# Optimization experiments

Measured on AMD Instinct MI355X. Metric: run time of the kernel, lower is better.

## Reference

```python
import jax, jax.numpy as jnp
import numpy as np

N = 100000   # nodes
E = 400000   # edges
G = 2048     # graphs in batch
H = 128      # hidden_channels
V = 100      # in_channels (element vocab)
L = 3        # hidden_layers (GAT)
LO = 2       # out_layers (dense)
SLOPE = 0.2  # GATConv negative_slope default


def setup_inputs() -> dict:
    key = jax.random.key(0)
    ks = jax.random.split(key, 14)
    s = 1.0 / np.sqrt(H)
    return {
        "x": jax.random.randint(ks[0], (N,), 0, V),
        "edge_index": jax.random.randint(ks[1], (2, E), 0, N),
        "edge_attr": jax.random.uniform(ks[2], (E, 1), dtype=jnp.float32),
        "batch": jnp.sort(jax.random.randint(ks[3], (N,), 0, G)),
        "emb": jax.random.normal(ks[4], (V, H), dtype=jnp.float32),
        "gat_W": jax.random.normal(ks[5], (L, H, H), dtype=jnp.float32) * s,
        "att_src": jax.random.normal(ks[6], (L, H), dtype=jnp.float32) * s,
        "att_dst": jax.random.normal(ks[7], (L, H), dtype=jnp.float32) * s,
        "edge_W": jax.random.normal(ks[8], (L, H), dtype=jnp.float32) * s,  # lin_edge: Linear(1, H, bias=False)
        "att_edge": jax.random.normal(ks[9], (L, H), dtype=jnp.float32) * s,
        "gat_b": jnp.zeros((L, H), dtype=jnp.float32),
        "lin_W": jax.random.normal(ks[10], (LO, H, H), dtype=jnp.float32) * s,
        "lin_b": jnp.zeros((LO, H), dtype=jnp.float32),
        "wp_W": jax.random.normal(ks[11], (H, 1), dtype=jnp.float32) * s,
        "wp_b": jnp.zeros((1,), dtype=jnp.float32),
    }


def _segment_softmax(logits, seg, num_segments):
    m = jax.ops.segment_max(logits, seg, num_segments=num_segments)
    e = jnp.exp(logits - m[seg])
    s = jax.ops.segment_sum(e, seg, num_segments=num_segments)
    return e / s[seg]


def reference(x, edge_index, edge_attr, batch, emb, gat_W, att_src, att_dst,
              edge_W, att_edge, gat_b, lin_W, lin_b, wp_W, wp_b):
    src, dst = edge_index[0], edge_index[1]
    # GATConv add_self_loops=True with fill_value='mean' for edge_attr
    loop = jnp.arange(N, dtype=src.dtype)
    src_sl = jnp.concatenate([src, loop])          # [E+N]
    dst_sl = jnp.concatenate([dst, loop])          # [E+N]
    ea_mean = jnp.mean(edge_attr, axis=0, keepdims=True)  # [1,1]
    ea_sl = jnp.concatenate([edge_attr, jnp.broadcast_to(ea_mean, (N, 1))], axis=0)  # [E+N,1]

    h = emb[x]  # [N,H]
    for l in range(L):
        xt = h @ gat_W[l]                 # shared lin_src/lin_dst, heads=1
        a_s = xt @ att_src[l]             # [N]
        a_d = xt @ att_dst[l]             # [N]
        a_e = (ea_sl * edge_W[l][None, :]) @ att_edge[l]  # lin_edge then att_edge: [E+N]
        alpha = jax.nn.leaky_relu(a_s[src_sl] + a_d[dst_sl] + a_e, negative_slope=SLOPE)
        alpha = _segment_softmax(alpha, dst_sl, N)
        out = jax.ops.segment_sum(xt[src_sl] * alpha[:, None], dst_sl, num_segments=N)
        out = out + gat_b[l]
        # F.normalize(h_x, 2, dim=1)
        nrm = jnp.linalg.norm(out, axis=1, keepdims=True)
        h = out / jnp.maximum(nrm, 1e-12)
    for i in range(LO):
        h = jax.nn.relu(h @ lin_W[i] + lin_b[i])
    m_x = jax.ops.segment_sum(h, batch, num_segments=G)  # scatter_sum readout [G,H]
    props = m_x @ wp_W + wp_b                            # [G,1]
    return jnp.squeeze(props, axis=1)                    # [G]
```

## Files before the change

### kernel.cpp

```cpp
#include <hip/hip_runtime.h>
#include <math.h>

#define N_NODES 100000
#define N_EDGES 400000
#define NG 2048
#define H 128
#define NV 100
#define NLAYERS 3
#define SLOPE 0.2f

#define SCAL_N 64

typedef __attribute__((ext_vector_type(8))) short bf16x8;
typedef __attribute__((ext_vector_type(4))) float f32x4;

__device__ __forceinline__ float wave_reduce_sum(float v){
  #pragma unroll
  for (int off = 32; off > 0; off >>= 1) v += __shfl_xor(v, off, 64);
  return v;
}
__device__ __forceinline__ unsigned short rne_bf16(float f){
  unsigned int u = __float_as_uint(f);
  u += 0x7FFF + ((u >> 16) & 1);
  return (unsigned short)(u >> 16);
}

#define PB_CONVW 320
#define PB_CONVE (PB_CONVW + 50)
#define PB_OUT   (PB_CONVE + 8)
#define PB_DOTS  (PB_OUT + 1)
#define PB_EASUM (PB_DOTS + 256)
#define PB_DEG   (PB_EASUM + 1954)
__global__ __launch_bounds__(256) void k_prep(
    const float* __restrict__ gat_W, const float* __restrict__ lin_W,
    unsigned short* __restrict__ Wf,
    const float* __restrict__ emb, unsigned short* __restrict__ embb,
    const float* __restrict__ ea, const float* __restrict__ ew,
    const float* __restrict__ ae, float* __restrict__ scal,
    const float* __restrict__ wp_b, float* __restrict__ out,
    const int* __restrict__ ei, int* __restrict__ deg)
{
  int b = blockIdx.x, tid = threadIdx.x;
  if (b < PB_CONVW){
    int i = b*256 + tid;
    int m   = i >> 14;
    int r   = i & 16383;
    int k0i = r >> 12;
    int r3  = r & 4095;
    int ct  = r3 >> 9;
    int r4  = r3 & 511;
    int lane= r4 >> 3;
    int j   = r4 & 7;
    int q = lane >> 4, ln = lane & 15;
    int k = k0i*32 + q*8 + j;
    int n = ct*16 + ln;
    const float* src = (m < 3) ? (gat_W + m*16384) : (lin_W + (m-3)*16384);
    Wf[i] = rne_bf16(src[k*H + n]);
  } else if (b < PB_CONVE){
    int i = (b - PB_CONVW)*256 + tid;
    if (i < NV*H) embb[i] = rne_bf16(emb[i]);
  } else if (b < PB_OUT){
    int g = (b - PB_CONVE)*256 + tid;
    if (g < NG) out[g] = wp_b[0];
  } else if (b < PB_DOTS){
    int l = tid >> 6, ln = tid & 63;
    if (l < NLAYERS){
      float p = ew[l*H + ln]*ae[l*H + ln] + ew[l*H + ln + 64]*ae[l*H + ln + 64];
      p = wave_reduce_sum(p);
      if (ln == 0) atomicAdd(&scal[32 + l], p);
    }
  } else if (b < PB_EASUM){
    int i = (b - PB_DOTS)*256 + tid;
    int stride = 256*256;
    float v = 0.f;
    for (; i < N_EDGES; i += stride) v += ea[i];
    v = wave_reduce_sum(v);
    if ((tid & 63) == 0) atomicAdd(&scal[0], v);
  } else {
    int i = (b - PB_EASUM)*256 + tid;
    if (i < N_EDGES + N_NODES){
      int d = (i < N_EDGES) ? ei[N_EDGES + i] : (i - N_EDGES);
      atomicAdd(&deg[d], 1);
    }
  }
}

__global__ __launch_bounds__(256) void k_alloc(
    const int* __restrict__ deg, int* __restrict__ row_ptr, int* __restrict__ counter){
  __shared__ int wsum[4];
  __shared__ int base;
  int n = blockIdx.x * 256 + threadIdx.x;
  int d = (n < N_NODES) ? deg[n] : 0;
  int lane = threadIdx.x & 63, wid = threadIdx.x >> 6;
  int v = d;
  #pragma unroll
  for (int off = 1; off < 64; off <<= 1){
    int u = __shfl_up(v, off, 64);
    if (lane >= off) v += u;
  }
  if (lane == 63) wsum[wid] = v;
  __syncthreads();
  if (threadIdx.x == 0){
    int t0 = wsum[0], t1 = wsum[1], t2 = wsum[2], t3 = wsum[3];
    base = atomicAdd(counter, t0 + t1 + t2 + t3);
    wsum[0] = 0; wsum[1] = t0; wsum[2] = t0 + t1; wsum[3] = t0 + t1 + t2;
  }
  __syncthreads();
  if (n < N_NODES) row_ptr[n] = base + wsum[wid] + (v - d);
}

__global__ void k_scatter(const int* __restrict__ ei, const float* __restrict__ ea,
                          const float* __restrict__ scal, const int* __restrict__ row_ptr,
                          int* __restrict__ cursor, int* __restrict__ csr_src,
                          float* __restrict__ csr_ea){
  int i = blockIdx.x * blockDim.x + threadIdx.x;
  if (i >= N_EDGES + N_NODES) return;
  int s, d; float v;
  if (i < N_EDGES){ s = ei[i]; d = ei[N_EDGES + i]; v = ea[i]; }
  else            { s = d = i - N_EDGES; v = scal[0] * (1.0f / N_EDGES); }
  int pos = row_ptr[d] + atomicAdd(&cursor[d], 1);
  csr_src[pos] = s;
  csr_ea[pos]  = v;
}

__global__ __launch_bounds__(256, 4) void k_gemm(
    const unsigned short* __restrict__ Ab, const int* __restrict__ xmap,
    const unsigned short* __restrict__ Wf,
    unsigned short* __restrict__ Cb,
    const float* __restrict__ att1, const float* __restrict__ att2,
    float* __restrict__ a_s_out, float* __restrict__ a_d_out,
    const float* __restrict__ bias,
    const int* __restrict__ batch, float* __restrict__ out,
    int mode)
{
  __shared__ unsigned short lw[16384];
  int tid  = threadIdx.x;
  int w    = tid >> 6;
  int lane = tid & 63;
  int q    = lane >> 4;
  int ln   = lane & 15;
  int waveRow = blockIdx.x*128 + w*32;

  #pragma unroll
  for (int i = 0; i < 8; ++i){
    int base = (i*256 + w*64) * 8;
    __builtin_amdgcn_global_load_lds(
        (const __attribute__((address_space(1))) unsigned int*)(Wf + base + lane*8),
        (__attribute__((address_space(3))) unsigned int*)(lw + base),
        16, 0, 0);
  }

  bf16x8 af[2][4];
  #pragma unroll
  for (int m = 0; m < 2; ++m){
    int r = waveRow + m*16 + ln;
    if (r >= N_NODES) r = N_NODES - 1;
    if (xmap) r = xmap[r];
    const unsigned short* Ar = Ab + (size_t)r*H;
    #pragma unroll
    for (int k0i = 0; k0i < 4; ++k0i)
      af[m][k0i] = *(const bf16x8*)(Ar + k0i*32 + q*8);
  }
  __syncthreads();

  f32x4 acc[2][8];
  #pragma unroll
  for (int m = 0; m < 2; ++m)
    #pragma unroll
    for (int ct = 0; ct < 8; ++ct) acc[m][ct] = (f32x4){0.f,0.f,0.f,0.f};

  #pragma unroll
  for (int k0i = 0; k0i < 4; ++k0i){
    #pragma unroll
    for (int ct = 0; ct < 8; ++ct){
      bf16x8 bw = *(const bf16x8*)(lw + k0i*4096 + ct*512 + lane*8);
      #pragma unroll
      for (int m = 0; m < 2; ++m)
        acc[m][ct] = __builtin_amdgcn_mfma_f32_16x16x32_bf16(af[m][k0i], bw, acc[m][ct], 0,0,0);
    }
  }

  if (mode == 0){
    float as_l[8], ad_l[8];
    #pragma unroll
    for (int ct = 0; ct < 8; ++ct){ as_l[ct] = att1[ct*16+ln]; ad_l[ct] = att2[ct*16+ln]; }
    #pragma unroll
    for (int m = 0; m < 2; ++m){
      #pragma unroll
      for (int r = 0; r < 4; ++r){
        int grow = waveRow + m*16 + q*4 + r;
        bool ok = grow < N_NODES;
        float ps = 0.f, pd = 0.f;
        #pragma unroll
        for (int ct = 0; ct < 8; ++ct){
          float v = acc[m][ct][r];
          if (ok) Cb[(size_t)grow*H + ct*16 + ln] = rne_bf16(v);
          ps += v * as_l[ct]; pd += v * ad_l[ct];
        }
        #pragma unroll
        for (int mk = 8; mk > 0; mk >>= 1){
          ps += __shfl_xor(ps, mk, 64);
          pd += __shfl_xor(pd, mk, 64);
        }
        if (ok && ln == 0){ a_s_out[grow] = ps; a_d_out[grow] = pd; }
      }
    }
  } else if (mode == 1){
    float b_l[8];
    #pragma unroll
    for (int ct = 0; ct < 8; ++ct) b_l[ct] = bias[ct*16+ln];
    #pragma unroll
    for (int m = 0; m < 2; ++m){
      #pragma unroll
      for (int r = 0; r < 4; ++r){
        int grow = waveRow + m*16 + q*4 + r;
        if (grow >= N_NODES) continue;
        #pragma unroll
        for (int ct = 0; ct < 8; ++ct)
          Cb[(size_t)grow*H + ct*16 + ln] = rne_bf16(fmaxf(acc[m][ct][r] + b_l[ct], 0.f));
      }
    }
  } else {
    float b_l[8], wp_l[8];
    #pragma unroll
    for (int ct = 0; ct < 8; ++ct){ b_l[ct] = bias[ct*16+ln]; wp_l[ct] = att1[ct*16+ln]; }
    #pragma unroll
    for (int m = 0; m < 2; ++m){
      #pragma unroll
      for (int r = 0; r < 4; ++r){
        int grow = waveRow + m*16 + q*4 + r;
        bool ok = grow < N_NODES;
        float ps = 0.f;
        #pragma unroll
        for (int ct = 0; ct < 8; ++ct)
          ps += fmaxf(acc[m][ct][r] + b_l[ct], 0.f) * wp_l[ct];
        #pragma unroll
        for (int mk = 8; mk > 0; mk >>= 1) ps += __shfl_xor(ps, mk, 64);
        if (ok && ln == 0) atomicAdd(&out[batch[grow]], ps);
      }
    }
  }
}

__global__ __launch_bounds__(256, 4) void k_aggregate(
    const uint2* __restrict__ xtb2, const float* __restrict__ a_s,
    const float* __restrict__ a_d, const int* __restrict__ csr_src,
    const float* __restrict__ csr_ea, const int* __restrict__ row_ptr,
    const int* __restrict__ deg, const float* __restrict__ scal, int l,
    const float* __restrict__ bias, uint2* __restrict__ hb2)
{
  __shared__ int2 lsw[4][2][32];
  int wid  = threadIdx.x >> 6;
  int lane = threadIdx.x & 63;
  int h    = lane >> 5;
  int c    = lane & 31;
  int n    = blockIdx.x*8 + wid*2 + h;
  if (n >= N_NODES) return;
  int beg = row_ptr[n];
  int d   = deg[n];
  float adn = a_d[n];
  float dl  = scal[32 + l];
  int maxd = max(d, __shfl_xor(d, 32, 64));

  float4 acc = make_float4(0.f,0.f,0.f,0.f);
  float ss = 0.f;
  for (int base = 0; base < maxd; base += 32){
    int s = 0; float wgt = 0.f;
    int j = base + c;
    if (j < d){
      int e = beg + j;
      s = csr_src[e];
      float lg = a_s[s] + adn + dl*csr_ea[e];
      lg = (lg > 0.f) ? lg : SLOPE*lg;
      wgt = __expf(lg);
    }
    int2 pk; pk.x = s; pk.y = __float_as_int(wgt);
    lsw[wid][h][c] = pk;

    int cnt8 = (min(32, maxd - base) + 7) & ~7;
    for (int j0 = 0; j0 < cnt8; j0 += 8){
      int2 sw[8];
      #pragma unroll
      for (int u = 0; u < 8; ++u) sw[u] = lsw[wid][h][j0 + u];
      uint2 xv[8];
      #pragma unroll
      for (int u = 0; u < 8; ++u)
        xv[u] = xtb2[(size_t)sw[u].x*(H/4) + c];
      #pragma unroll
      for (int u = 0; u < 8; ++u){
        float wgt8 = __int_as_float(sw[u].y);
        float x0 = __uint_as_float(xv[u].x << 16);
        float x1 = __uint_as_float(xv[u].x & 0xFFFF0000u);
        float x2 = __uint_as_float(xv[u].y << 16);
        float x3 = __uint_as_float(xv[u].y & 0xFFFF0000u);
        ss    += wgt8;
        acc.x += wgt8 * x0;
        acc.y += wgt8 * x1;
        acc.z += wgt8 * x2;
        acc.w += wgt8 * x3;
      }
    }
  }

  float4 bv = *(const float4*)(bias + c*4);
  float inv = 1.0f / ss;
  acc.x = acc.x*inv + bv.x;
  acc.y = acc.y*inv + bv.y;
  acc.z = acc.z*inv + bv.z;
  acc.w = acc.w*inv + bv.w;
  float sq = acc.x*acc.x + acc.y*acc.y + acc.z*acc.z + acc.w*acc.w;
  #pragma unroll
  for (int off = 16; off > 0; off >>= 1) sq += __shfl_xor(sq, off, 64);
  float rn = 1.0f / fmaxf(sqrtf(sq), 1e-12f);
  uint2 o;
  o.x = ((unsigned int)rne_bf16(acc.y*rn) << 16) | rne_bf16(acc.x*rn);
  o.y = ((unsigned int)rne_bf16(acc.w*rn) << 16) | rne_bf16(acc.z*rn);
  hb2[(size_t)n*(H/4) + c] = o;
}

extern "C" void kernel_launch(void* const* d_in, const int* in_sizes, int n_in,
                              void* d_out, int out_size, void* d_ws, size_t ws_size,
                              hipStream_t stream) {
  const int*   x          = (const int*)  d_in[0];
  const int*   edge_index = (const int*)  d_in[1];
  const float* edge_attr  = (const float*)d_in[2];
  const int*   batch      = (const int*)  d_in[3];
  const float* emb        = (const float*)d_in[4];
  const float* gat_W      = (const float*)d_in[5];
  const float* att_src    = (const float*)d_in[6];
  const float* att_dst    = (const float*)d_in[7];
  const float* edge_W     = (const float*)d_in[8];
  const float* att_edge   = (const float*)d_in[9];
  const float* gat_b      = (const float*)d_in[10];
  const float* lin_W      = (const float*)d_in[11];
  const float* lin_b      = (const float*)d_in[12];
  const float* wp_W       = (const float*)d_in[13];
  const float* wp_b       = (const float*)d_in[14];
  float* out = (float*)d_out;

  unsigned short* hb  = (unsigned short*)d_ws;
  unsigned short* xtb = hb + (size_t)N_NODES*H;
  unsigned short* Wt  = xtb + (size_t)N_NODES*H;
  unsigned short* embb= Wt + 5*16384;
  float* a_s    = (float*)(embb + NV*H);
  float* a_d    = a_s + N_NODES;
  float* csr_ea = a_d + N_NODES;
  float* scal   = csr_ea + (N_EDGES + N_NODES);
  int*   deg    = (int*)(scal + SCAL_N);
  int*   cursor = deg + N_NODES;
  int*   row_ptr= cursor + N_NODES;
  int*   csr_src= row_ptr + N_NODES;

  hipMemsetAsync(scal, 0, (size_t)(SCAL_N + 2*N_NODES) * sizeof(float), stream);

  k_prep<<<PB_DEG, 256, 0, stream>>>(
      gat_W, lin_W, Wt, emb, embb, edge_attr, edge_W, att_edge, scal,
      wp_b, out, edge_index, deg);
  k_alloc<<<(N_NODES + 255)/256, 256, 0, stream>>>(deg, row_ptr, (int*)&scal[48]);
  k_scatter<<<(N_EDGES + N_NODES + 255)/256, 256, 0, stream>>>(
      edge_index, edge_attr, scal, row_ptr, cursor, csr_src, csr_ea);

  const int gemm_grid = (N_NODES + 127) / 128;
  for (int l = 0; l < NLAYERS; ++l){
    k_gemm<<<gemm_grid, 256, 0, stream>>>(
        (l == 0) ? embb : hb, (l == 0) ? x : nullptr,
        Wt + (size_t)l*16384, xtb,
        att_src + l*H, att_dst + l*H, a_s, a_d,
        nullptr, nullptr, nullptr, 0);
    k_aggregate<<<(N_NODES + 7)/8, 256, 0, stream>>>(
        (const uint2*)xtb, a_s, a_d, csr_src, csr_ea, row_ptr, deg,
        scal, l, gat_b + l*H, (uint2*)hb);
  }
  k_gemm<<<gemm_grid, 256, 0, stream>>>(
      hb, nullptr, Wt + (size_t)3*16384, xtb,
      nullptr, nullptr, nullptr, nullptr, lin_b, nullptr, nullptr, 1);
  k_gemm<<<gemm_grid, 256, 0, stream>>>(
      xtb, nullptr, Wt + (size_t)4*16384, nullptr,
      wp_W, nullptr, nullptr, nullptr, lin_b + H, batch, out, 2);
}
```

Measured before the change: 325.6 us.

## Fuse dense MLP layers into one kernel and reuse degree-count ranks for CSR scatter

The two dense layers plus the readout now run in one kernel. The intermediate activation stays in swizzled LDS, so it is no longer written to and reread from global memory as bf16. Separately, the rank returned by the degree-count atomic is stored per edge, which removes the second atomic cursor pass in the scatter and the cursor memset. The cost is more LDS per block and lower occupancy (launch bounds 2), plus an extra rank array of size E+N.

```diff
diff --git a/kernel.cpp b/kernel.cpp
--- a/kernel.cpp
+++ b/kernel.cpp
@@ -38,7 +38,8 @@
     const float* __restrict__ ea, const float* __restrict__ ew,
     const float* __restrict__ ae, float* __restrict__ scal,
     const float* __restrict__ wp_b, float* __restrict__ out,
-    const int* __restrict__ ei, int* __restrict__ deg)
+    const int* __restrict__ ei, int* __restrict__ deg,
+    int* __restrict__ rank)
 {
   int b = blockIdx.x, tid = threadIdx.x;
   if (b < PB_CONVW){
@@ -80,7 +81,7 @@
     int i = (b - PB_EASUM)*256 + tid;
     if (i < N_EDGES + N_NODES){
       int d = (i < N_EDGES) ? ei[N_EDGES + i] : (i - N_EDGES);
-      atomicAdd(&deg[d], 1);
+      rank[i] = atomicAdd(&deg[d], 1);
     }
   }
 }
@@ -111,14 +112,14 @@
 
 __global__ void k_scatter(const int* __restrict__ ei, const float* __restrict__ ea,
                           const float* __restrict__ scal, const int* __restrict__ row_ptr,
-                          int* __restrict__ cursor, int* __restrict__ csr_src,
+                          const int* __restrict__ rank, int* __restrict__ csr_src,
                           float* __restrict__ csr_ea){
   int i = blockIdx.x * blockDim.x + threadIdx.x;
   if (i >= N_EDGES + N_NODES) return;
   int s, d; float v;
   if (i < N_EDGES){ s = ei[i]; d = ei[N_EDGES + i]; v = ea[i]; }
   else            { s = d = i - N_EDGES; v = scal[0] * (1.0f / N_EDGES); }
-  int pos = row_ptr[d] + atomicAdd(&cursor[d], 1);
+  int pos = row_ptr[d] + rank[i];
   csr_src[pos] = s;
   csr_ea[pos]  = v;
 }
@@ -128,10 +129,7 @@
     const unsigned short* __restrict__ Wf,
     unsigned short* __restrict__ Cb,
     const float* __restrict__ att1, const float* __restrict__ att2,
-    float* __restrict__ a_s_out, float* __restrict__ a_d_out,
-    const float* __restrict__ bias,
-    const int* __restrict__ batch, float* __restrict__ out,
-    int mode)
+    float* __restrict__ a_s_out, float* __restrict__ a_d_out)
 {
   __shared__ unsigned short lw[16384];
   int tid  = threadIdx.x;
@@ -180,64 +178,152 @@
     }
   }
 
-  if (mode == 0){
-    float as_l[8], ad_l[8];
-    #pragma unroll
-    for (int ct = 0; ct < 8; ++ct){ as_l[ct] = att1[ct*16+ln]; ad_l[ct] = att2[ct*16+ln]; }
-    #pragma unroll
-    for (int m = 0; m < 2; ++m){
-      #pragma unroll
-      for (int r = 0; r < 4; ++r){
-        int grow = waveRow + m*16 + q*4 + r;
-        bool ok = grow < N_NODES;
-        float ps = 0.f, pd = 0.f;
-        #pragma unroll
-        for (int ct = 0; ct < 8; ++ct){
-          float v = acc[m][ct][r];
-          if (ok) Cb[(size_t)grow*H + ct*16 + ln] = rne_bf16(v);
-          ps += v * as_l[ct]; pd += v * ad_l[ct];
-        }
-        #pragma unroll
-        for (int mk = 8; mk > 0; mk >>= 1){
-          ps += __shfl_xor(ps, mk, 64);
-          pd += __shfl_xor(pd, mk, 64);
-        }
-        if (ok && ln == 0){ a_s_out[grow] = ps; a_d_out[grow] = pd; }
+  float as_l[8], ad_l[8];
+  #pragma unroll
+  for (int ct = 0; ct < 8; ++ct){ as_l[ct] = att1[ct*16+ln]; ad_l[ct] = att2[ct*16+ln]; }
+  #pragma unroll
+  for (int m = 0; m < 2; ++m){
+    #pragma unroll
+    for (int r = 0; r < 4; ++r){
+      int grow = waveRow + m*16 + q*4 + r;
+      bool ok = grow < N_NODES;
+      float ps = 0.f, pd = 0.f;
+      #pragma unroll
+      for (int ct = 0; ct < 8; ++ct){
+        float v = acc[m][ct][r];
+        if (ok) Cb[(size_t)grow*H + ct*16 + ln] = rne_bf16(v);
+        ps += v * as_l[ct]; pd += v * ad_l[ct];
       }
-    }
-  } else if (mode == 1){
-    float b_l[8];
-    #pragma unroll
-    for (int ct = 0; ct < 8; ++ct) b_l[ct] = bias[ct*16+ln];
-    #pragma unroll
-    for (int m = 0; m < 2; ++m){
-      #pragma unroll
-      for (int r = 0; r < 4; ++r){
-        int grow = waveRow + m*16 + q*4 + r;
-        if (grow >= N_NODES) continue;
-        #pragma unroll
-        for (int ct = 0; ct < 8; ++ct)
-          Cb[(size_t)grow*H + ct*16 + ln] = rne_bf16(fmaxf(acc[m][ct][r] + b_l[ct], 0.f));
+      #pragma unroll
+      for (int mk = 8; mk > 0; mk >>= 1){
+        ps += __shfl_xor(ps, mk, 64);
+        pd += __shfl_xor(pd, mk, 64);
       }
-    }
-  } else {
-    float b_l[8], wp_l[8];
-    #pragma unroll
-    for (int ct = 0; ct < 8; ++ct){ b_l[ct] = bias[ct*16+ln]; wp_l[ct] = att1[ct*16+ln]; }
-    #pragma unroll
-    for (int m = 0; m < 2; ++m){
-      #pragma unroll
-      for (int r = 0; r < 4; ++r){
-        int grow = waveRow + m*16 + q*4 + r;
-        bool ok = grow < N_NODES;
-        float ps = 0.f;
-        #pragma unroll
-        for (int ct = 0; ct < 8; ++ct)
-          ps += fmaxf(acc[m][ct][r] + b_l[ct], 0.f) * wp_l[ct];
-        #pragma unroll
-        for (int mk = 8; mk > 0; mk >>= 1) ps += __shfl_xor(ps, mk, 64);
-        if (ok && ln == 0) atomicAdd(&out[batch[grow]], ps);
+      if (ok && ln == 0){ a_s_out[grow] = ps; a_d_out[grow] = pd; }
+    }
+  }
+}
+
+__global__ __launch_bounds__(256, 2) void k_dense(
+    const unsigned short* __restrict__ Ab,
+    const unsigned short* __restrict__ Wf,
+    const float* __restrict__ b1, const float* __restrict__ b2,
+    const float* __restrict__ wp, const int* __restrict__ batch,
+    float* __restrict__ out)
+{
+  __shared__ unsigned short lw[16384];
+  __shared__ unsigned short lh[16384];
+  int tid  = threadIdx.x;
+  int w    = tid >> 6;
+  int lane = tid & 63;
+  int q    = lane >> 4;
+  int ln   = lane & 15;
+  int waveRow = blockIdx.x*128 + w*32;
+
+  #pragma unroll
+  for (int i = 0; i < 8; ++i){
+    int base = (i*256 + w*64) * 8;
+    __builtin_amdgcn_global_load_lds(
+        (const __attribute__((address_space(1))) unsigned int*)(Wf + base + lane*8),
+        (__attribute__((address_space(3))) unsigned int*)(lw + base),
+        16, 0, 0);
+  }
+  bf16x8 af[2][4];
+  #pragma unroll
+  for (int m = 0; m < 2; ++m){
+    int r = waveRow + m*16 + ln;
+    if (r >= N_NODES) r = N_NODES - 1;
+    const unsigned short* Ar = Ab + (size_t)r*H;
+    #pragma unroll
+    for (int k0i = 0; k0i < 4; ++k0i)
+      af[m][k0i] = *(const bf16x8*)(Ar + k0i*32 + q*8);
+  }
+  __syncthreads();
+
+  f32x4 acc[2][8];
+  #pragma unroll
+  for (int m = 0; m < 2; ++m)
+    #pragma unroll
+    for (int ct = 0; ct < 8; ++ct) acc[m][ct] = (f32x4){0.f,0.f,0.f,0.f};
+  #pragma unroll
+  for (int k0i = 0; k0i < 4; ++k0i){
+    #pragma unroll
+    for (int ct = 0; ct < 8; ++ct){
+      bf16x8 bw = *(const bf16x8*)(lw + k0i*4096 + ct*512 + lane*8);
+      #pragma unroll
+      for (int m = 0; m < 2; ++m)
+        acc[m][ct] = __builtin_amdgcn_mfma_f32_16x16x32_bf16(af[m][k0i], bw, acc[m][ct], 0,0,0);
+    }
+  }
+
+  float b1_l[8];
+  #pragma unroll
+  for (int ct = 0; ct < 8; ++ct) b1_l[ct] = b1[ct*16+ln];
+  #pragma unroll
+  for (int m = 0; m < 2; ++m){
+    #pragma unroll
+    for (int r = 0; r < 4; ++r){
+      int lr = w*32 + m*16 + q*4 + r;
+      int sw = (lr & 7) << 3;
+      #pragma unroll
+      for (int ct = 0; ct < 8; ++ct){
+        int col = ct*16 + ln;
+        lh[lr*128 + (col ^ sw)] = rne_bf16(fmaxf(acc[m][ct][r] + b1_l[ct], 0.f));
       }
+    }
+  }
+  __syncthreads();
+
+  #pragma unroll
+  for (int i = 0; i < 8; ++i){
+    int base = (i*256 + w*64) * 8;
+    __builtin_amdgcn_global_load_lds(
+        (const __attribute__((address_space(1))) unsigned int*)(Wf + 16384 + base + lane*8),
+        (__attribute__((address_space(3))) unsigned int*)(lw + base),
+        16, 0, 0);
+  }
+  bf16x8 af2[2][4];
+  #pragma unroll
+  for (int m = 0; m < 2; ++m){
+    int lr = w*32 + m*16 + ln;
+    int sw = (lr & 7) << 3;
+    #pragma unroll
+    for (int k0i = 0; k0i < 4; ++k0i)
+      af2[m][k0i] = *(const bf16x8*)(lh + lr*128 + ((k0i*32 + q*8) ^ sw));
+  }
+  __syncthreads();
+
+  #pragma unroll
+  for (int m = 0; m < 2; ++m)
+    #pragma unroll
+    for (int ct = 0; ct < 8; ++ct) acc[m][ct] = (f32x4){0.f,0.f,0.f,0.f};
+  #pragma unroll
+  for (int k0i = 0; k0i < 4; ++k0i){
+    #pragma unroll
+    for (int ct = 0; ct < 8; ++ct){
+      bf16x8 bw = *(const bf16x8*)(lw + k0i*4096 + ct*512 + lane*8);
+      #pragma unroll
+      for (int m = 0; m < 2; ++m)
+        acc[m][ct] = __builtin_amdgcn_mfma_f32_16x16x32_bf16(af2[m][k0i], bw, acc[m][ct], 0,0,0);
+    }
+  }
+
+  float b2_l[8], wp_l[8];
+  #pragma unroll
+  for (int ct = 0; ct < 8; ++ct){ b2_l[ct] = b2[ct*16+ln]; wp_l[ct] = wp[ct*16+ln]; }
+  #pragma unroll
+  for (int m = 0; m < 2; ++m){
+    #pragma unroll
+    for (int r = 0; r < 4; ++r){
+      int grow = waveRow + m*16 + q*4 + r;
+      bool ok = grow < N_NODES;
+      float ps = 0.f;
+      #pragma unroll
+      for (int ct = 0; ct < 8; ++ct)
+        ps += fmaxf(acc[m][ct][r] + b2_l[ct], 0.f) * wp_l[ct];
+      #pragma unroll
+      for (int mk = 8; mk > 0; mk >>= 1) ps += __shfl_xor(ps, mk, 64);
+      if (ok && ln == 0) atomicAdd(&out[batch[grow]], ps);
     }
   }
 }
@@ -347,34 +433,29 @@
   float* csr_ea = a_d + N_NODES;
   float* scal   = csr_ea + (N_EDGES + N_NODES);
   int*   deg    = (int*)(scal + SCAL_N);
-  int*   cursor = deg + N_NODES;
-  int*   row_ptr= cursor + N_NODES;
+  int*   rank   = deg + N_NODES;
+  int*   row_ptr= rank + (N_EDGES + N_NODES);
   int*   csr_src= row_ptr + N_NODES;
 
-  hipMemsetAsync(scal, 0, (size_t)(SCAL_N + 2*N_NODES) * sizeof(float), stream);
+  hipMemsetAsync(scal, 0, (size_t)(SCAL_N + N_NODES) * sizeof(float), stream);
 
   k_prep<<<PB_DEG, 256, 0, stream>>>(
       gat_W, lin_W, Wt, emb, embb, edge_attr, edge_W, att_edge, scal,
-      wp_b, out, edge_index, deg);
+      wp_b, out, edge_index, deg, rank);
   k_alloc<<<(N_NODES + 255)/256, 256, 0, stream>>>(deg, row_ptr, (int*)&scal[48]);
   k_scatter<<<(N_EDGES + N_NODES + 255)/256, 256, 0, stream>>>(
-      edge_index, edge_attr, scal, row_ptr, cursor, csr_src, csr_ea);
+      edge_index, edge_attr, scal, row_ptr, rank, csr_src, csr_ea);
 
   const int gemm_grid = (N_NODES + 127) / 128;
   for (int l = 0; l < NLAYERS; ++l){
     k_gemm<<<gemm_grid, 256, 0, stream>>>(
         (l == 0) ? embb : hb, (l == 0) ? x : nullptr,
         Wt + (size_t)l*16384, xtb,
-        att_src + l*H, att_dst + l*H, a_s, a_d,
-        nullptr, nullptr, nullptr, 0);
+        att_src + l*H, att_dst + l*H, a_s, a_d);
     k_aggregate<<<(N_NODES + 7)/8, 256, 0, stream>>>(
         (const uint2*)xtb, a_s, a_d, csr_src, csr_ea, row_ptr, deg,
         scal, l, gat_b + l*H, (uint2*)hb);
   }
-  k_gemm<<<gemm_grid, 256, 0, stream>>>(
-      hb, nullptr, Wt + (size_t)3*16384, xtb,
-      nullptr, nullptr, nullptr, nullptr, lin_b, nullptr, nullptr, 1);
-  k_gemm<<<gemm_grid, 256, 0, stream>>>(
-      xtb, nullptr, Wt + (size_t)4*16384, nullptr,
-      wp_W, nullptr, nullptr, nullptr, lin_b + H, batch, out, 2);
-}
+  k_dense<<<gemm_grid, 256, 0, stream>>>(
+      hb, Wt + (size_t)3*16384, lin_b, lin_b + H, wp_W, batch, out);
+}
```

New measurement: 318.1 us. 1.02x faster.
